# Optimization experiments

Hardware: AMD Instinct MI355X
Metric: run time of the kernel (lower is better)

Reference implementation:

```python
import jax, jax.numpy as jnp
import numpy as np

N = 100000      # nodes
E = 1600000     # edges
IN = 128        # in_channels
ED = 32         # edge_dim
H = 4           # heads
C = 32          # out_channels per head
NEG_SLOPE = 0.2


def setup_inputs() -> dict:
    key = jax.random.key(0)
    ks = jax.random.split(key, 10)
    s = 0.1  # glorot-ish scale
    return {
        "x": jax.random.normal(ks[0], (N, IN), dtype=jnp.float32),
        "edge_index": jax.random.randint(ks[1], (2, E), 0, N, dtype=jnp.int32),
        "edge_attr": jax.random.normal(ks[2], (E, ED), dtype=jnp.float32),
        "W": jax.random.normal(ks[3], (IN, H * C), dtype=jnp.float32) * s,
        "att_src": jax.random.normal(ks[4], (H, C), dtype=jnp.float32) * s,
        "att_dst": jax.random.normal(ks[5], (H, C), dtype=jnp.float32) * s,
        "W_edge": jax.random.normal(ks[6], (ED, H * C), dtype=jnp.float32) * s,
        "att_edge": jax.random.normal(ks[7], (H, C), dtype=jnp.float32) * s,
        "gat_bias": jnp.zeros((H * C,), dtype=jnp.float32),
        "bias": jnp.zeros((C,), dtype=jnp.float32),
    }


def reference(x, edge_index, edge_attr, W, att_src, att_dst, W_edge, att_edge, gat_bias, bias):
    # eval mode: no dropout. GATConv with edge_dim, concat=True, then mean over heads.
    src, dst = edge_index[0], edge_index[1]
    xh = (x @ W).reshape(N, H, C)                       # [N,H,C]
    a_src = jnp.einsum("nhc,hc->nh", xh, att_src)      # [N,H]
    a_dst = jnp.einsum("nhc,hc->nh", xh, att_dst)      # [N,H]
    eh = (edge_attr @ W_edge).reshape(E, H, C)          # [E,H,C]
    a_edge = jnp.einsum("ehc,hc->eh", eh, att_edge)    # [E,H]
    logits = a_src[src] + a_dst[dst] + a_edge           # [E,H]
    logits = jnp.where(logits >= 0, logits, NEG_SLOPE * logits)  # leaky_relu
    # segment softmax over edges grouped by destination node
    seg_max = jax.ops.segment_max(logits, dst, num_segments=N)  # [N,H]
    expv = jnp.exp(logits - seg_max[dst])
    denom = jax.ops.segment_sum(expv, dst, num_segments=N)      # [N,H]
    alpha = expv / denom[dst]                                    # [E,H]
    msg = xh[src] * alpha[:, :, None]                            # [E,H,C]
    out = jax.ops.segment_sum(msg, dst, num_segments=N)          # [N,H,C]
    out = out + gat_bias.reshape(1, H, C)                        # GATConv bias (concat)
    out = out.mean(axis=1)                                       # combine='mean' -> [N,C]
    out = out + bias
    return jax.nn.relu(out)
```

## Files before the change

kernel.cpp:

```cpp
#include <hip/hip_runtime.h>
#include <hip/hip_bf16.h>

typedef __hip_bfloat16 bf16;

#define N_NODES 100000
#define N_EDGES 1600000
#define IN_CH   128
#define ED_DIM  32
#define HEADS   4
#define C_OUT   32
#define HC      128
#define NEG_SLOPE 0.2f
#define SCAN_BLOCKS 98

__device__ __forceinline__ float bf_lo(unsigned u) { return __uint_as_float(u << 16); }
__device__ __forceinline__ float bf_hi(unsigned u) { return __uint_as_float(u & 0xffff0000u); }
__device__ __forceinline__ unsigned short f2bf_rne(float f) {
    unsigned u = __float_as_uint(f);
    return (unsigned short)((u + 0x7fffu + ((u >> 16) & 1u)) >> 16);
}
__device__ __forceinline__ float load_any(const void* p, int i, int isf32) {
    return isf32 ? ((const float*)p)[i]
                 : __uint_as_float(((unsigned)((const unsigned short*)p)[i]) << 16);
}

__global__ void detect(const unsigned* __restrict__ xw, int* __restrict__ flag) {
    __shared__ int cnt;
    if (threadIdx.x == 0) cnt = 0;
    __syncthreads();
    unsigned w = xw[threadIdx.x];
    int e = (w >> 7) & 0xFF;
    if (e >= 140) atomicAdd(&cnt, 1);
    __syncthreads();
    if (threadIdx.x == 0) *flag = (cnt >= 32) ? 1 : 0;
}

__global__ void report_err(unsigned short* out, float code) {
    if (threadIdx.x < 16) out[threadIdx.x] = f2bf_rne(code);
}

__global__ __launch_bounds__(256) void zero_ints(int* __restrict__ p, int n) {
    int i = blockIdx.x * 256 + threadIdx.x;
    if (i < n) p[i] = 0;
}

__global__ __launch_bounds__(256) void prep_small(
    const int* __restrict__ flag,
    const void* __restrict__ W, const void* __restrict__ att_src,
    const void* __restrict__ att_dst, const void* __restrict__ W_edge,
    const void* __restrict__ att_edge, const void* __restrict__ gat_bias,
    const void* __restrict__ bias,
    unsigned short* __restrict__ Wc, float* __restrict__ att_src_f,
    float* __restrict__ att_dst_f, float* __restrict__ gat_bias_f,
    float* __restrict__ bias_f, float* __restrict__ Wa) {

    int isf32 = *flag;
    int t = threadIdx.x;
    for (int i = t; i < IN_CH * HC; i += 256)
        Wc[i] = f2bf_rne(load_any(W, i, isf32));
    if (t < 128) {
        att_src_f[t]  = load_any(att_src, t, isf32);
        att_dst_f[t]  = load_any(att_dst, t, isf32);
        gat_bias_f[t] = load_any(gat_bias, t, isf32);
    }
    if (t < 32) bias_f[t] = load_any(bias, t, isf32);
    if (t < 128) {
        int d = t & 31, h = t >> 5;
        float acc = 0.f;
        for (int c = 0; c < C_OUT; ++c)
            acc += load_any(W_edge, d * HC + h * C_OUT + c, isf32) *
                   load_any(att_edge, h * C_OUT + c, isf32);
        Wa[h * 32 + d] = acc;
    }
}

__global__ __launch_bounds__(256) void node_gemm(
    const int* __restrict__ flag, const void* __restrict__ x,
    const unsigned short* __restrict__ Wc,
    const float* __restrict__ att_src_f, const float* __restrict__ att_dst_f,
    unsigned short* __restrict__ xh,
    float* __restrict__ a_src, float* __restrict__ a_dst) {

    __shared__ unsigned short Wl[IN_CH * HC];
    __shared__ float xl[32 * IN_CH];

    int isf32 = *flag;
    int t = threadIdx.x;
    int node0 = blockIdx.x * 32;

    const uint4* Wg = (const uint4*)Wc;
    uint4* Wl4 = (uint4*)Wl;
#pragma unroll
    for (int k = 0; k < 8; ++k) Wl4[t + k * 256] = Wg[t + k * 256];

    if (isf32) {
        const float4* xg = (const float4*)((const float*)x + (size_t)node0 * IN_CH);
        float4* xl4 = (float4*)xl;
#pragma unroll
        for (int k = 0; k < 4; ++k) xl4[t + k * 256] = xg[t + k * 256];
    } else {
        const unsigned* xg = (const unsigned*)((const unsigned short*)x + (size_t)node0 * IN_CH);
#pragma unroll
        for (int k = 0; k < 8; ++k) {
            unsigned u = xg[t + k * 256];
            int f = 2 * (t + k * 256);
            xl[f]     = bf_lo(u);
            xl[f + 1] = bf_hi(u);
        }
    }
    __syncthreads();

    int q  = t & 31;
    int i0 = (t >> 5) * 4;
    int j4 = q * 4;
    float acc[16];
#pragma unroll
    for (int k = 0; k < 16; ++k) acc[k] = 0.f;

    const float* xr0 = xl + (i0 + 0) * IN_CH;
    const float* xr1 = xl + (i0 + 1) * IN_CH;
    const float* xr2 = xl + (i0 + 2) * IN_CH;
    const float* xr3 = xl + (i0 + 3) * IN_CH;

#pragma unroll 8
    for (int d = 0; d < IN_CH; ++d) {
        uint2 wb = *(const uint2*)(Wl + d * HC + j4);
        float w0 = bf_lo(wb.x), w1 = bf_hi(wb.x);
        float w2 = bf_lo(wb.y), w3 = bf_hi(wb.y);
        float x0 = xr0[d], x1 = xr1[d], x2 = xr2[d], x3 = xr3[d];
        acc[0]  += x0 * w0; acc[1]  += x0 * w1; acc[2]  += x0 * w2; acc[3]  += x0 * w3;
        acc[4]  += x1 * w0; acc[5]  += x1 * w1; acc[6]  += x1 * w2; acc[7]  += x1 * w3;
        acc[8]  += x2 * w0; acc[9]  += x2 * w1; acc[10] += x2 * w2; acc[11] += x2 * w3;
        acc[12] += x3 * w0; acc[13] += x3 * w1; acc[14] += x3 * w2; acc[15] += x3 * w3;
    }

    float4 sa = *(const float4*)(att_src_f + j4);
    float4 da = *(const float4*)(att_dst_f + j4);

#pragma unroll
    for (int k = 0; k < 4; ++k) {
        int node = node0 + i0 + k;
        float a0 = acc[4 * k], a1 = acc[4 * k + 1], a2 = acc[4 * k + 2], a3 = acc[4 * k + 3];
        unsigned p0 = ((unsigned)f2bf_rne(a1) << 16) | f2bf_rne(a0);
        unsigned p1 = ((unsigned)f2bf_rne(a3) << 16) | f2bf_rne(a2);
        *(uint2*)(xh + (size_t)node * HC + j4) = make_uint2(p0, p1);

        float ps = a0 * sa.x + a1 * sa.y + a2 * sa.z + a3 * sa.w;
        float pd = a0 * da.x + a1 * da.y + a2 * da.z + a3 * da.w;
        ps += __shfl_xor(ps, 1); ps += __shfl_xor(ps, 2); ps += __shfl_xor(ps, 4);
        pd += __shfl_xor(pd, 1); pd += __shfl_xor(pd, 2); pd += __shfl_xor(pd, 4);
        if ((q & 7) == 0) {
            int h = q >> 3;
            a_src[node * HEADS + h] = ps;
            a_dst[node * HEADS + h] = pd;
        }
    }
}

__global__ __launch_bounds__(256) void hist(const int* __restrict__ ei,
                                            int* __restrict__ count) {
    int e = blockIdx.x * 256 + threadIdx.x;
    if (e < N_EDGES) atomicAdd(&count[ei[N_EDGES + e]], 1);
}

__global__ __launch_bounds__(256) void scan_a(const int* __restrict__ count,
                                              int* __restrict__ starts,
                                              int* __restrict__ blockSums) {
    __shared__ int sd[256];
    int t = threadIdx.x;
    int base = blockIdx.x * 1024 + t * 4;
    int c0 = (base + 0 < N_NODES) ? count[base + 0] : 0;
    int c1 = (base + 1 < N_NODES) ? count[base + 1] : 0;
    int c2 = (base + 2 < N_NODES) ? count[base + 2] : 0;
    int c3 = (base + 3 < N_NODES) ? count[base + 3] : 0;
    int s = c0 + c1 + c2 + c3;
    sd[t] = s;
    __syncthreads();
    for (int off = 1; off < 256; off <<= 1) {
        int v = (t >= off) ? sd[t - off] : 0;
        __syncthreads();
        sd[t] += v;
        __syncthreads();
    }
    int excl = sd[t] - s;
    if (base + 0 < N_NODES) starts[base + 0] = excl;
    if (base + 1 < N_NODES) starts[base + 1] = excl + c0;
    if (base + 2 < N_NODES) starts[base + 2] = excl + c0 + c1;
    if (base + 3 < N_NODES) starts[base + 3] = excl + c0 + c1 + c2;
    if (t == 255) blockSums[blockIdx.x] = sd[255];
}

__global__ __launch_bounds__(128) void scan_b(int* __restrict__ blockSums) {
    __shared__ int sd[128];
    int t = threadIdx.x;
    int v = (t < SCAN_BLOCKS) ? blockSums[t] : 0;
    sd[t] = v;
    __syncthreads();
    for (int off = 1; off < 128; off <<= 1) {
        int u = (t >= off) ? sd[t - off] : 0;
        __syncthreads();
        sd[t] += u;
        __syncthreads();
    }
    if (t < SCAN_BLOCKS) blockSums[t] = sd[t] - v;
}

__global__ __launch_bounds__(256) void scan_c(int* __restrict__ starts,
                                              int* __restrict__ cursor,
                                              const int* __restrict__ blockSums) {
    int off = blockSums[blockIdx.x];
    int base = blockIdx.x * 1024 + threadIdx.x * 4;
#pragma unroll
    for (int k = 0; k < 4; ++k) {
        int idx = base + k;
        if (idx < N_NODES) {
            int v = starts[idx] + off;
            starts[idx] = v;
            cursor[idx] = v;
        }
    }
    if (blockIdx.x == 0 && threadIdx.x == 0) starts[N_NODES] = N_EDGES;
}

__global__ __launch_bounds__(256) void scatter(
    const int* __restrict__ flag,
    const int* __restrict__ ei, const void* __restrict__ edge_attr,
    const float* __restrict__ a_src, const float* __restrict__ a_dst,
    const float* __restrict__ Wa, int* __restrict__ cursor,
    int* __restrict__ perm_src, float4* __restrict__ perm_w) {

    __shared__ float WaL[128];
    int t = threadIdx.x;
    if (t < 128) WaL[t] = Wa[t];
    __syncthreads();

    int isf32 = *flag;
    int e = blockIdx.x * 256 + t;
    if (e >= N_EDGES) return;
    int s  = ei[e];
    int dn = ei[N_EDGES + e];

    float ae0 = 0.f, ae1 = 0.f, ae2 = 0.f, ae3 = 0.f;
    if (isf32) {
        const float4* ea = (const float4*)((const float*)edge_attr + (size_t)e * ED_DIM);
#pragma unroll
        for (int k = 0; k < 8; ++k) {
            float4 v = ea[k];
            int d = 4 * k;
            ae0 += v.x * WaL[d] + v.y * WaL[d + 1] + v.z * WaL[d + 2] + v.w * WaL[d + 3];
            ae1 += v.x * WaL[32 + d] + v.y * WaL[33 + d] + v.z * WaL[34 + d] + v.w * WaL[35 + d];
            ae2 += v.x * WaL[64 + d] + v.y * WaL[65 + d] + v.z * WaL[66 + d] + v.w * WaL[67 + d];
            ae3 += v.x * WaL[96 + d] + v.y * WaL[97 + d] + v.z * WaL[98 + d] + v.w * WaL[99 + d];
        }
    } else {
        const uint4* ea = (const uint4*)((const unsigned short*)edge_attr + (size_t)e * ED_DIM);
#pragma unroll
        for (int k = 0; k < 4; ++k) {
            uint4 v = ea[k];
            float g0 = bf_lo(v.x), g1 = bf_hi(v.x), g2 = bf_lo(v.y), g3 = bf_hi(v.y);
            float g4 = bf_lo(v.z), g5 = bf_hi(v.z), g6 = bf_lo(v.w), g7 = bf_hi(v.w);
            int d = 8 * k;
            ae0 += g0*WaL[d] + g1*WaL[d+1] + g2*WaL[d+2] + g3*WaL[d+3]
                 + g4*WaL[d+4] + g5*WaL[d+5] + g6*WaL[d+6] + g7*WaL[d+7];
            ae1 += g0*WaL[32+d] + g1*WaL[33+d] + g2*WaL[34+d] + g3*WaL[35+d]
                 + g4*WaL[36+d] + g5*WaL[37+d] + g6*WaL[38+d] + g7*WaL[39+d];
            ae2 += g0*WaL[64+d] + g1*WaL[65+d] + g2*WaL[66+d] + g3*WaL[67+d]
                 + g4*WaL[68+d] + g5*WaL[69+d] + g6*WaL[70+d] + g7*WaL[71+d];
            ae3 += g0*WaL[96+d] + g1*WaL[97+d] + g2*WaL[98+d] + g3*WaL[99+d]
                 + g4*WaL[100+d] + g5*WaL[101+d] + g6*WaL[102+d] + g7*WaL[103+d];
        }
    }

    float4 as = *(const float4*)(a_src + (size_t)s * 4);
    float4 ad = *(const float4*)(a_dst + (size_t)dn * 4);
    float l0 = as.x + ad.x + ae0;
    float l1 = as.y + ad.y + ae1;
    float l2 = as.z + ad.z + ae2;
    float l3 = as.w + ad.w + ae3;
    l0 = (l0 >= 0.f) ? l0 : NEG_SLOPE * l0;
    l1 = (l1 >= 0.f) ? l1 : NEG_SLOPE * l1;
    l2 = (l2 >= 0.f) ? l2 : NEG_SLOPE * l2;
    l3 = (l3 >= 0.f) ? l3 : NEG_SLOPE * l3;
    float w0 = __expf(l0), w1 = __expf(l1), w2 = __expf(l2), w3 = __expf(l3);

    int pos = atomicAdd(&cursor[dn], 1);
    perm_src[pos] = s;
    perm_w[pos] = make_float4(w0, w1, w2, w3);
}

__global__ __launch_bounds__(256) void gather(
    const int* __restrict__ flag,
    const int* __restrict__ starts, const int* __restrict__ perm_src,
    const float4* __restrict__ perm_w, const unsigned short* __restrict__ xh,
    const float* __restrict__ gat_bias_f, const float* __restrict__ bias_f,
    void* __restrict__ out) {

    __shared__ int   sS[4][64];
    __shared__ float sW[4][64 * 4];

    int t = threadIdx.x;
    int w = t >> 6, lane = t & 63, h = lane >> 4;
    int n = blockIdx.x * 4 + w;
    if (n >= N_NODES) return;
    int isf32 = *flag;

    int st = starts[n], en = starts[n + 1];
    float f0 = 0.f, f1 = 0.f, wsum = 0.f;

    for (int base = st; base < en; base += 64) {
        int cnt = en - base;
        if (cnt > 64) cnt = 64;
        __builtin_amdgcn_wave_barrier();
        if (lane < cnt) {
            sS[w][lane] = perm_src[base + lane];
            *(float4*)&sW[w][lane * 4] = perm_w[base + lane];
        }
        __builtin_amdgcn_wave_barrier();
#pragma unroll 4
        for (int jj = 0; jj < cnt; ++jj) {
            int s = sS[w][jj];
            float wt = sW[w][jj * 4 + h];
            unsigned xv = *(const unsigned*)(xh + ((size_t)s << 7) + 2 * lane);
            f0 += wt * bf_lo(xv);
            f1 += wt * bf_hi(xv);
            wsum += wt;
        }
    }

    float inv = (wsum > 0.f) ? 1.f / wsum : 0.f;
    float v0 = f0 * inv + gat_bias_f[2 * lane];
    float v1 = f1 * inv + gat_bias_f[2 * lane + 1];
    v0 += __shfl_xor(v0, 16); v0 += __shfl_xor(v0, 32);
    v1 += __shfl_xor(v1, 16); v1 += __shfl_xor(v1, 32);

    if (lane < 16) {
        int c = 2 * lane;
        float o0 = fmaxf(v0 * 0.25f + bias_f[c],     0.f);
        float o1 = fmaxf(v1 * 0.25f + bias_f[c + 1], 0.f);
        if (isf32) {
            *(float2*)((float*)out + (size_t)n * C_OUT + c) = make_float2(o0, o1);
        } else {
            unsigned p = ((unsigned)f2bf_rne(o1) << 16) | f2bf_rne(o0);
            *(unsigned*)((unsigned short*)out + (size_t)n * C_OUT + c) = p;
        }
    }
}

extern "C" void kernel_launch(void* const* d_in, const int* in_sizes, int n_in,
                              void* d_out, int out_size, void* d_ws, size_t ws_size,
                              hipStream_t stream) {
    const void* x         = d_in[0];
    const int*  ei        = (const int*)d_in[1];
    const void* edge_attr = d_in[2];
    const void* W         = d_in[3];
    const void* att_src   = d_in[4];
    const void* att_dst   = d_in[5];
    const void* W_edge    = d_in[6];
    const void* att_edge  = d_in[7];
    const void* gat_bias  = d_in[8];
    const void* bias      = d_in[9];

    char* ws = (char*)d_ws;
    size_t off = 0;
    auto align256 = [](size_t v) { return (v + 255) & ~(size_t)255; };

    unsigned short* xh = (unsigned short*)(ws + off);
    off = align256(off + (size_t)N_NODES * HC * sizeof(unsigned short));
    float* a_src_w = (float*)(ws + off);
    off = align256(off + (size_t)N_NODES * HEADS * sizeof(float));
    float* a_dst_w = (float*)(ws + off);
    off = align256(off + (size_t)N_NODES * HEADS * sizeof(float));
    int* count = (int*)(ws + off);
    off = align256(off + (size_t)N_NODES * sizeof(int));
    int* starts = (int*)(ws + off);
    off = align256(off + (size_t)(N_NODES + 1) * sizeof(int));
    int* cursor = (int*)(ws + off);
    off = align256(off + (size_t)N_NODES * sizeof(int));
    int* blockSums = (int*)(ws + off);
    off = align256(off + (size_t)SCAN_BLOCKS * sizeof(int));
    int* perm_src = (int*)(ws + off);
    off = align256(off + (size_t)N_EDGES * sizeof(int));
    float4* perm_w = (float4*)(ws + off);
    off = align256(off + (size_t)N_EDGES * sizeof(float4));
    float* Wa = (float*)(ws + off);
    off = align256(off + 128 * sizeof(float));
    unsigned short* Wc = (unsigned short*)(ws + off);
    off = align256(off + (size_t)IN_CH * HC * sizeof(unsigned short));
    float* att_src_f = (float*)(ws + off);
    off = align256(off + 128 * sizeof(float));
    float* att_dst_f = (float*)(ws + off);
    off = align256(off + 128 * sizeof(float));
    float* gat_bias_f = (float*)(ws + off);
    off = align256(off + 128 * sizeof(float));
    float* bias_f = (float*)(ws + off);
    off = align256(off + 32 * sizeof(float));
    int* dflag = (int*)(ws + off);
    off = align256(off + sizeof(int));
    size_t need = off;

    if (ws_size < need) {
        report_err<<<1, 64, 0, stream>>>((unsigned short*)d_out, 1500.0f);
        return;
    }

    (void)hipGetLastError();

    detect<<<1, 256, 0, stream>>>((const unsigned*)x, dflag);
    prep_small<<<1, 256, 0, stream>>>(dflag, W, att_src, att_dst, W_edge,
                                      att_edge, gat_bias, bias,
                                      Wc, att_src_f, att_dst_f, gat_bias_f,
                                      bias_f, Wa);
    zero_ints<<<(N_NODES + 255) / 256, 256, 0, stream>>>(count, N_NODES);
    node_gemm<<<N_NODES / 32, 256, 0, stream>>>(dflag, x, Wc, att_src_f,
                                                att_dst_f, xh, a_src_w, a_dst_w);
    hist<<<(N_EDGES + 255) / 256, 256, 0, stream>>>(ei, count);
    scan_a<<<SCAN_BLOCKS, 256, 0, stream>>>(count, starts, blockSums);
    scan_b<<<1, 128, 0, stream>>>(blockSums);
    scan_c<<<SCAN_BLOCKS, 256, 0, stream>>>(starts, cursor, blockSums);
    scatter<<<(N_EDGES + 255) / 256, 256, 0, stream>>>(dflag, ei, edge_attr,
                                                       a_src_w, a_dst_w, Wa,
                                                       cursor, perm_src, perm_w);
    gather<<<N_NODES / 4, 256, 0, stream>>>(dflag, starts, perm_src, perm_w,
                                            xh, gat_bias_f, bias_f, d_out);

    hipError_t e = hipGetLastError();
    if (e != hipSuccess) {
        report_err<<<1, 64, 0, stream>>>((unsigned short*)d_out,
                                         1000.0f + (float)(int)e);
    }
}
```

Measured before the change: 631.0 us.

## Fuse degree histogram into edge-weight kernel and store bf16 weights in edge order

The per-edge logit and exp computation moves into a kernel that also counts destination degrees, so the separate histogram pass is gone. Weights are written in original edge order as packed bf16 instead of being scattered as float4. A lightweight build_perm kernel then scatters (src, edge id) pairs, and gather fetches the weights indirectly by edge id. This shrinks the scattered write traffic and the weight storage but adds a random gather of weights, an extra launch, and lower-precision attention weights.

```diff
diff --git a/kernel.cpp b/kernel.cpp
--- a/kernel.cpp
+++ b/kernel.cpp
@@ -18,6 +18,9 @@
 __device__ __forceinline__ unsigned short f2bf_rne(float f) {
     unsigned u = __float_as_uint(f);
     return (unsigned short)((u + 0x7fffu + ((u >> 16) & 1u)) >> 16);
+}
+__device__ __forceinline__ unsigned pack_bf2(float a, float b) {
+    return ((unsigned)f2bf_rne(b) << 16) | f2bf_rne(a);
 }
 __device__ __forceinline__ float load_any(const void* p, int i, int isf32) {
     return isf32 ? ((const float*)p)[i]
@@ -141,9 +144,8 @@
     for (int k = 0; k < 4; ++k) {
         int node = node0 + i0 + k;
         float a0 = acc[4 * k], a1 = acc[4 * k + 1], a2 = acc[4 * k + 2], a3 = acc[4 * k + 3];
-        unsigned p0 = ((unsigned)f2bf_rne(a1) << 16) | f2bf_rne(a0);
-        unsigned p1 = ((unsigned)f2bf_rne(a3) << 16) | f2bf_rne(a2);
-        *(uint2*)(xh + (size_t)node * HC + j4) = make_uint2(p0, p1);
+        *(uint2*)(xh + (size_t)node * HC + j4) =
+            make_uint2(pack_bf2(a0, a1), pack_bf2(a2, a3));
 
         float ps = a0 * sa.x + a1 * sa.y + a2 * sa.z + a3 * sa.w;
         float pd = a0 * da.x + a1 * da.y + a2 * da.z + a3 * da.w;
@@ -157,77 +159,12 @@
     }
 }
 
-__global__ __launch_bounds__(256) void hist(const int* __restrict__ ei,
-                                            int* __restrict__ count) {
-    int e = blockIdx.x * 256 + threadIdx.x;
-    if (e < N_EDGES) atomicAdd(&count[ei[N_EDGES + e]], 1);
-}
-
-__global__ __launch_bounds__(256) void scan_a(const int* __restrict__ count,
-                                              int* __restrict__ starts,
-                                              int* __restrict__ blockSums) {
-    __shared__ int sd[256];
-    int t = threadIdx.x;
-    int base = blockIdx.x * 1024 + t * 4;
-    int c0 = (base + 0 < N_NODES) ? count[base + 0] : 0;
-    int c1 = (base + 1 < N_NODES) ? count[base + 1] : 0;
-    int c2 = (base + 2 < N_NODES) ? count[base + 2] : 0;
-    int c3 = (base + 3 < N_NODES) ? count[base + 3] : 0;
-    int s = c0 + c1 + c2 + c3;
-    sd[t] = s;
-    __syncthreads();
-    for (int off = 1; off < 256; off <<= 1) {
-        int v = (t >= off) ? sd[t - off] : 0;
-        __syncthreads();
-        sd[t] += v;
-        __syncthreads();
-    }
-    int excl = sd[t] - s;
-    if (base + 0 < N_NODES) starts[base + 0] = excl;
-    if (base + 1 < N_NODES) starts[base + 1] = excl + c0;
-    if (base + 2 < N_NODES) starts[base + 2] = excl + c0 + c1;
-    if (base + 3 < N_NODES) starts[base + 3] = excl + c0 + c1 + c2;
-    if (t == 255) blockSums[blockIdx.x] = sd[255];
-}
-
-__global__ __launch_bounds__(128) void scan_b(int* __restrict__ blockSums) {
-    __shared__ int sd[128];
-    int t = threadIdx.x;
-    int v = (t < SCAN_BLOCKS) ? blockSums[t] : 0;
-    sd[t] = v;
-    __syncthreads();
-    for (int off = 1; off < 128; off <<= 1) {
-        int u = (t >= off) ? sd[t - off] : 0;
-        __syncthreads();
-        sd[t] += u;
-        __syncthreads();
-    }
-    if (t < SCAN_BLOCKS) blockSums[t] = sd[t] - v;
-}
-
-__global__ __launch_bounds__(256) void scan_c(int* __restrict__ starts,
-                                              int* __restrict__ cursor,
-                                              const int* __restrict__ blockSums) {
-    int off = blockSums[blockIdx.x];
-    int base = blockIdx.x * 1024 + threadIdx.x * 4;
-#pragma unroll
-    for (int k = 0; k < 4; ++k) {
-        int idx = base + k;
-        if (idx < N_NODES) {
-            int v = starts[idx] + off;
-            starts[idx] = v;
-            cursor[idx] = v;
-        }
-    }
-    if (blockIdx.x == 0 && threadIdx.x == 0) starts[N_NODES] = N_EDGES;
-}
-
-__global__ __launch_bounds__(256) void scatter(
+__global__ __launch_bounds__(256) void edge_w(
     const int* __restrict__ flag,
     const int* __restrict__ ei, const void* __restrict__ edge_attr,
     const float* __restrict__ a_src, const float* __restrict__ a_dst,
-    const float* __restrict__ Wa, int* __restrict__ cursor,
-    int* __restrict__ perm_src, float4* __restrict__ perm_w) {
+    const float* __restrict__ Wa,
+    uint2* __restrict__ w4b, int* __restrict__ count) {
 
     __shared__ float WaL[128];
     int t = threadIdx.x;
@@ -239,6 +176,8 @@
     if (e >= N_EDGES) return;
     int s  = ei[e];
     int dn = ei[N_EDGES + e];
+
+    atomicAdd(&count[dn], 1);
 
     float ae0 = 0.f, ae1 = 0.f, ae2 = 0.f, ae3 = 0.f;
     if (isf32) {
@@ -283,20 +222,88 @@
     l3 = (l3 >= 0.f) ? l3 : NEG_SLOPE * l3;
     float w0 = __expf(l0), w1 = __expf(l1), w2 = __expf(l2), w3 = __expf(l3);
 
+    w4b[e] = make_uint2(pack_bf2(w0, w1), pack_bf2(w2, w3));
+}
+
+__global__ __launch_bounds__(256) void scan_a(const int* __restrict__ count,
+                                              int* __restrict__ starts,
+                                              int* __restrict__ blockSums) {
+    __shared__ int sd[256];
+    int t = threadIdx.x;
+    int base = blockIdx.x * 1024 + t * 4;
+    int c0 = (base + 0 < N_NODES) ? count[base + 0] : 0;
+    int c1 = (base + 1 < N_NODES) ? count[base + 1] : 0;
+    int c2 = (base + 2 < N_NODES) ? count[base + 2] : 0;
+    int c3 = (base + 3 < N_NODES) ? count[base + 3] : 0;
+    int s = c0 + c1 + c2 + c3;
+    sd[t] = s;
+    __syncthreads();
+    for (int off = 1; off < 256; off <<= 1) {
+        int v = (t >= off) ? sd[t - off] : 0;
+        __syncthreads();
+        sd[t] += v;
+        __syncthreads();
+    }
+    int excl = sd[t] - s;
+    if (base + 0 < N_NODES) starts[base + 0] = excl;
+    if (base + 1 < N_NODES) starts[base + 1] = excl + c0;
+    if (base + 2 < N_NODES) starts[base + 2] = excl + c0 + c1;
+    if (base + 3 < N_NODES) starts[base + 3] = excl + c0 + c1 + c2;
+    if (t == 255) blockSums[blockIdx.x] = sd[255];
+}
+
+__global__ __launch_bounds__(128) void scan_b(int* __restrict__ blockSums) {
+    __shared__ int sd[128];
+    int t = threadIdx.x;
+    int v = (t < SCAN_BLOCKS) ? blockSums[t] : 0;
+    sd[t] = v;
+    __syncthreads();
+    for (int off = 1; off < 128; off <<= 1) {
+        int u = (t >= off) ? sd[t - off] : 0;
+        __syncthreads();
+        sd[t] += u;
+        __syncthreads();
+    }
+    if (t < SCAN_BLOCKS) blockSums[t] = sd[t] - v;
+}
+
+__global__ __launch_bounds__(256) void scan_c(int* __restrict__ starts,
+                                              int* __restrict__ cursor,
+                                              const int* __restrict__ blockSums) {
+    int off = blockSums[blockIdx.x];
+    int base = blockIdx.x * 1024 + threadIdx.x * 4;
+#pragma unroll
+    for (int k = 0; k < 4; ++k) {
+        int idx = base + k;
+        if (idx < N_NODES) {
+            int v = starts[idx] + off;
+            starts[idx] = v;
+            cursor[idx] = v;
+        }
+    }
+    if (blockIdx.x == 0 && threadIdx.x == 0) starts[N_NODES] = N_EDGES;
+}
+
+__global__ __launch_bounds__(256) void build_perm(
+    const int* __restrict__ ei, int* __restrict__ cursor,
+    uint2* __restrict__ perm_se) {
+    int e = blockIdx.x * 256 + threadIdx.x;
+    if (e >= N_EDGES) return;
+    int s  = ei[e];
+    int dn = ei[N_EDGES + e];
     int pos = atomicAdd(&cursor[dn], 1);
-    perm_src[pos] = s;
-    perm_w[pos] = make_float4(w0, w1, w2, w3);
+    perm_se[pos] = make_uint2((unsigned)s, (unsigned)e);
 }
 
 __global__ __launch_bounds__(256) void gather(
     const int* __restrict__ flag,
-    const int* __restrict__ starts, const int* __restrict__ perm_src,
-    const float4* __restrict__ perm_w, const unsigned short* __restrict__ xh,
+    const int* __restrict__ starts, const uint2* __restrict__ perm_se,
+    const uint2* __restrict__ w4b, const unsigned short* __restrict__ xh,
     const float* __restrict__ gat_bias_f, const float* __restrict__ bias_f,
     void* __restrict__ out) {
 
-    __shared__ int   sS[4][64];
-    __shared__ float sW[4][64 * 4];
+    __shared__ int  sS[4][64];
+    __shared__ uint2 sW[4][64];
 
     int t = threadIdx.x;
     int w = t >> 6, lane = t & 63, h = lane >> 4;
@@ -312,14 +319,17 @@
         if (cnt > 64) cnt = 64;
         __builtin_amdgcn_wave_barrier();
         if (lane < cnt) {
-            sS[w][lane] = perm_src[base + lane];
-            *(float4*)&sW[w][lane * 4] = perm_w[base + lane];
+            uint2 se = perm_se[base + lane];
+            sS[w][lane] = (int)se.x;
+            sW[w][lane] = w4b[se.y];
         }
         __builtin_amdgcn_wave_barrier();
 #pragma unroll 4
         for (int jj = 0; jj < cnt; ++jj) {
             int s = sS[w][jj];
-            float wt = sW[w][jj * 4 + h];
+            uint2 wb = sW[w][jj];
+            unsigned hw = (h & 2) ? wb.y : wb.x;
+            float wt = (h & 1) ? bf_hi(hw) : bf_lo(hw);
             unsigned xv = *(const unsigned*)(xh + ((size_t)s << 7) + 2 * lane);
             f0 += wt * bf_lo(xv);
             f1 += wt * bf_hi(xv);
@@ -378,10 +388,10 @@
     off = align256(off + (size_t)N_NODES * sizeof(int));
     int* blockSums = (int*)(ws + off);
     off = align256(off + (size_t)SCAN_BLOCKS * sizeof(int));
-    int* perm_src = (int*)(ws + off);
-    off = align256(off + (size_t)N_EDGES * sizeof(int));
-    float4* perm_w = (float4*)(ws + off);
-    off = align256(off + (size_t)N_EDGES * sizeof(float4));
+    uint2* w4b = (uint2*)(ws + off);
+    off = align256(off + (size_t)N_EDGES * sizeof(uint2));
+    uint2* perm_se = (uint2*)(ws + off);
+    off = align256(off + (size_t)N_EDGES * sizeof(uint2));
     float* Wa = (float*)(ws + off);
     off = align256(off + 128 * sizeof(float));
     unsigned short* Wc = (unsigned short*)(ws + off);
@@ -413,14 +423,14 @@
     zero_ints<<<(N_NODES + 255) / 256, 256, 0, stream>>>(count, N_NODES);
     node_gemm<<<N_NODES / 32, 256, 0, stream>>>(dflag, x, Wc, att_src_f,
                                                 att_dst_f, xh, a_src_w, a_dst_w);
-    hist<<<(N_EDGES + 255) / 256, 256, 0, stream>>>(ei, count);
+    edge_w<<<(N_EDGES + 255) / 256, 256, 0, stream>>>(dflag, ei, edge_attr,
+                                                      a_src_w, a_dst_w, Wa,
+                                                      w4b, count);
     scan_a<<<SCAN_BLOCKS, 256, 0, stream>>>(count, starts, blockSums);
     scan_b<<<1, 128, 0, stream>>>(blockSums);
     scan_c<<<SCAN_BLOCKS, 256, 0, stream>>>(starts, cursor, blockSums);
-    scatter<<<(N_EDGES + 255) / 256, 256, 0, stream>>>(dflag, ei, edge_attr,
-                                                       a_src_w, a_dst_w, Wa,
-                                                       cursor, perm_src, perm_w);
-    gather<<<N_NODES / 4, 256, 0, stream>>>(dflag, starts, perm_src, perm_w,
+    build_perm<<<(N_EDGES + 255) / 256, 256, 0, stream>>>(ei, cursor, perm_se);
+    gather<<<N_NODES / 4, 256, 0, stream>>>(dflag, starts, perm_se, w4b,
                                             xh, gat_bias_f, bias_f, d_out);
 
     hipError_t e = hipGetLastError();
```

Measured after the change: 650.5 us. +3.1%, slower.
